# Kernel optimization log

Hardware: AMD Instinct MI355X
Metric: run time of the kernel (lower is better)

The kernel has to match this reference:

```python
import jax, jax.numpy as jnp
import numpy as np
from math import sqrt

EMA_W = 0.3  # ema_weight
LN_EPS = 1e-5


def setup_inputs() -> dict:
    key = jax.random.key(0)
    ks = jax.random.split(key, 16)
    B, L, H, E = 8, 1024, 8, 64
    d_ff, dp_rank = 2048, 8
    inp = {
        "queries": jax.random.normal(ks[0], (B, L, H, E), jnp.float32),
        "keys": jax.random.normal(ks[1], (B, L, H, E), jnp.float32),
        "values": jax.random.normal(ks[2], (B, L, H, E), jnp.float32),
        "attn_mask": jnp.zeros((B, 1, L, L), jnp.bool_),
        # dynamic-projection mlp: Linear(E, dp_rank)
        "mlp_w": jax.random.normal(ks[3], (E, dp_rank), jnp.float32) / sqrt(E),
        "mlp_b": jnp.zeros((dp_rank,), jnp.float32),
        # ff_1: Linear(E,d_ff) -> GELU -> Linear(d_ff,E)
        "ff1_w1": jax.random.normal(ks[4], (E, d_ff), jnp.float32) / sqrt(E),
        "ff1_b1": jnp.zeros((d_ff,), jnp.float32),
        "ff1_w2": jax.random.normal(ks[5], (d_ff, E), jnp.float32) / sqrt(d_ff),
        "ff1_b2": jnp.zeros((E,), jnp.float32),
        # ff_2
        "ff2_w1": jax.random.normal(ks[6], (E, d_ff), jnp.float32) / sqrt(E),
        "ff2_b1": jnp.zeros((d_ff,), jnp.float32),
        "ff2_w2": jax.random.normal(ks[7], (d_ff, E), jnp.float32) / sqrt(d_ff),
        "ff2_b2": jnp.zeros((E,), jnp.float32),
        # LayerNorm(E)
        "ln_w": jnp.ones((E,), jnp.float32),
        "ln_b": jnp.zeros((E,), jnp.float32),
    }
    return inp


def _dynamic_projection(src, mlp_w, mlp_b):
    # src: [B,L,H,E] -> softmax over dp_rank, then einsum 'blhe,blhr->blhe'
    sm = jax.nn.softmax(src @ mlp_w + mlp_b, axis=-1)  # [B,L,H,R]
    return jnp.einsum('blhe,blhr->blhe', src, sm)


def _ffn(x, w1, b1, w2, b2):
    return jax.nn.gelu(x @ w1 + b1, approximate=False) @ w2 + b2


def reference(queries, keys, values, attn_mask,
              mlp_w, mlp_b,
              ff1_w1, ff1_b1, ff1_w2, ff1_b2,
              ff2_w1, ff2_b1, ff2_w2, ff2_b2,
              ln_w, ln_b):
    E = queries.shape[-1]
    scale = 1.0 / sqrt(24.0)   # hardcoded in source
    scale1 = 1.0 / sqrt(E)

    dp_values = _dynamic_projection(values, mlp_w, mlp_b)
    dp_keys = _dynamic_projection(keys, mlp_w, mlp_b)

    # ema state starts at zeros every forward, so ema = (1-w) * x
    ema_queries = (1.0 - EMA_W) * queries
    ema_keys = (1.0 - EMA_W) * dp_keys

    # NOTE: source masks a scores tensor that is then overwritten; mask has
    # no effect on the output, so attn_mask is unused (kept for fidelity).
    scores = jnp.einsum('blhe,bshe->bhls', ema_queries, ema_keys)
    scores1 = jnp.einsum('blhe,bshe->bhls', queries, keys)

    A = jax.nn.softmax(scale * scores, axis=-1)    # dropout = identity (eval)
    A1 = jax.nn.softmax(scale1 * scores1, axis=-1)

    V = jnp.einsum('bhls,bshd->blhd', A, dp_values)
    V1 = jnp.einsum('bhls,bshd->blhd', A1, values)

    src = _ffn(V, ff1_w1, ff1_b1, ff1_w2, ff1_b2) + _ffn(V1, ff2_w1, ff2_b1, ff2_w2, ff2_b2)

    mu = jnp.mean(src, axis=-1, keepdims=True)
    var = jnp.mean(jnp.square(src - mu), axis=-1, keepdims=True)
    out = (src - mu) * jax.lax.rsqrt(var + LN_EPS) * ln_w + ln_b
    return out
```

## Files before the change

### kernel.cpp

```cpp
#include <hip/hip_runtime.h>

typedef _Float16 f16x8 __attribute__((ext_vector_type(8)));
typedef _Float16 f16x2 __attribute__((ext_vector_type(2)));
typedef float f32x4 __attribute__((ext_vector_type(4)));
typedef float f32x16 __attribute__((ext_vector_type(16)));
typedef unsigned short u16x8 __attribute__((ext_vector_type(8)));
typedef unsigned int u32x4 __attribute__((ext_vector_type(4)));

static __device__ __forceinline__ unsigned short f2h(float x) {
  return __builtin_bit_cast(unsigned short, (_Float16)x);
}
static __device__ __forceinline__ float h2f(unsigned short u) {
  return (float)__builtin_bit_cast(_Float16, u);
}

static __device__ __forceinline__ f16x2 gelu_pk(f16x2 x) {
  const f16x2 P4 = {(_Float16)4.0f, (_Float16)4.0f};
  const f16x2 N4 = {(_Float16)-4.0f, (_Float16)-4.0f};
  const f16x2 C1 = {(_Float16)0.392761f, (_Float16)0.392761f};
  const f16x2 C3 = {(_Float16)-0.0512736f, (_Float16)-0.0512736f};
  const f16x2 C5 = {(_Float16)0.00376322f, (_Float16)0.00376322f};
  const f16x2 C7 = {(_Float16)-0.000100287f, (_Float16)-0.000100287f};
  const f16x2 HF = {(_Float16)0.5f, (_Float16)0.5f};
  const f16x2 ONE = {(_Float16)1.0f, (_Float16)1.0f};
  const f16x2 ZRO = {(_Float16)0.0f, (_Float16)0.0f};
  f16x2 xc = __builtin_elementwise_max(__builtin_elementwise_min(x, P4), N4);
  f16x2 u = xc * xc;
  f16x2 p = __builtin_elementwise_fma(
      __builtin_elementwise_fma(__builtin_elementwise_fma(C7, u, C5), u, C3),
      u, C1);
  f16x2 q = __builtin_elementwise_fma(xc, p, HF);
  f16x2 qc = __builtin_elementwise_max(__builtin_elementwise_min(q, ONE), ZRO);
  return x * qc;
}

static __device__ __forceinline__ int sig16(int v) {
  return (v & ~12) | ((v & 4) << 1) | ((v & 8) >> 1);
}

__global__ __launch_bounds__(256) void k_prep(
    const float* __restrict__ vsrc, const float* __restrict__ ksrc,
    const float* __restrict__ w11, const float* __restrict__ w21,
    const float* __restrict__ w12, const float* __restrict__ w22,
    unsigned short* __restrict__ vtb, unsigned short* __restrict__ kf16,
    unsigned short* __restrict__ w1t1, unsigned short* __restrict__ w2t1,
    unsigned short* __restrict__ w1t2, unsigned short* __restrict__ w2t2) {
  int bid = blockIdx.x, tid = threadIdx.x;
  if (bid >= 1152) {
    int kb = bid - 1152, bh = kb >> 4, lt = kb & 15, b = bh >> 3, h = bh & 7;
    const float* src = ksrc + (((b * 1024 + lt * 64) * 8 + h) << 6);
    unsigned short* dst = kf16 + bh * 65536 + lt * 4096;
#pragma unroll
    for (int i = 0; i < 2; ++i) {
      int c = tid + i * 256, r = c >> 3, c8 = c & 7;
      const float* s = src + r * 512 + c8 * 8;
      f32x4 a = *(const f32x4*)s, b4 = *(const f32x4*)(s + 4);
      u16x8 vv;
#pragma unroll
      for (int j = 0; j < 4; ++j) { vv[j] = f2h(a[j]); vv[j + 4] = f2h(b4[j]); }
      int off = ((c8 >> 2) * 4 + (r >> 4)) * 512 + ((c8 & 3) * 16 + (r & 15)) * 8;
      *(u16x8*)(dst + off) = vv;
    }
    return;
  }
  __shared__ unsigned short t[64][72];
  const float* src; unsigned short* dst; int srs, drs = 0;
  bool isw2 = false, isv = false;
  if (bid < 1024) {
    int bh = bid >> 4, lt = bid & 15, b = bh >> 3, h = bh & 7;
    src = vsrc + (((b * 1024 + lt * 64) * 8 + h) << 6); srs = 512;
    dst = vtb + bh * 65536 + lt * 4096; isv = true;
  } else {
    int wb = bid - 1024, which = wb >> 5, ti = wb & 31;
    isw2 = (which & 1);
    if (which == 0)      { src = w11 + ti * 64;   srs = 2048; dst = w1t1 + ti * 4096; drs = 64; }
    else if (which == 1) { src = w21 + ti * 4096; srs = 64;   dst = w2t1 + ti * 64;   drs = 2048; }
    else if (which == 2) { src = w12 + ti * 64;   srs = 2048; dst = w1t2 + ti * 4096; drs = 64; }
    else                 { src = w22 + ti * 4096; srs = 64;   dst = w2t2 + ti * 64;   drs = 2048; }
  }
#pragma unroll
  for (int i = 0; i < 2; ++i) {
    int c = tid + i * 256, r = c >> 3, c0 = (c & 7) * 8;
    const float* s = src + r * srs + c0;
    int tr = isw2 ? sig16(r) : r;
#pragma unroll
    for (int j = 0; j < 8; ++j) t[c0 + j][tr] = f2h(s[j]);
  }
  __syncthreads();
#pragma unroll
  for (int i = 0; i < 2; ++i) {
    int c = tid + i * 256, r = c >> 3, c8 = c & 7;
    u16x8 vv;
#pragma unroll
    for (int j = 0; j < 8; ++j) vv[j] = t[r][c8 * 8 + j];
    int off = isv ? ((c8 >> 2) * 4 + (r >> 4)) * 512 + ((c8 & 3) * 16 + (r & 15)) * 8
                  : r * drs + c8 * 8;
    *(u16x8*)(dst + off) = vv;
  }
}

__global__ __launch_bounds__(64) __attribute__((amdgpu_waves_per_eu(1, 2)))
void k_attn(
    const float* __restrict__ q, const unsigned short* __restrict__ kf16,
    const unsigned short* __restrict__ vtb,
    unsigned short* __restrict__ Vo, unsigned short* __restrict__ V1o) {
  int bid = blockIdx.x;
  int swz = (bid & 7) * 256 + (bid >> 3);
  int bh = swz >> 5, rb = swz & 31;
  int b = bh >> 3, h = bh & 7;
  int lane = threadIdx.x & 63, t = lane & 15, g = lane >> 4;

  __shared__ unsigned short Pl[2][2048];

  f16x8 aq[2][2];
#pragma unroll
  for (int sub = 0; sub < 2; ++sub) {
    int row = rb * 32 + sub * 16 + t;
    const float* qp = q + ((b * 1024 + row) * 8 + h) * 64;
#pragma unroll
    for (int ks = 0; ks < 2; ++ks) {
      f32x4 q0 = *(const f32x4*)(qp + ks * 32 + g * 8);
      f32x4 q1 = *(const f32x4*)(qp + ks * 32 + g * 8 + 4);
      f16x8 a;
#pragma unroll
      for (int j = 0; j < 4; ++j) { a[j] = (_Float16)q0[j]; a[j + 4] = (_Float16)q1[j]; }
      aq[sub][ks] = a;
    }
  }

  const float scl[2] = {0.14429954f, 0.18033688f};
  float lsp[2][2][4];
  f32x4 o[2][2][4];
#pragma unroll
  for (int v = 0; v < 2; ++v)
#pragma unroll
    for (int sub = 0; sub < 2; ++sub)
#pragma unroll
      for (int i = 0; i < 4; ++i) {
        lsp[v][sub][i] = 0.f;
        o[v][sub][i] = (f32x4){0, 0, 0, 0};
      }

  const unsigned short* kfb = kf16 + bh * 65536;
  const unsigned short* vbase = vtb + bh * 65536;

  f16x8 bk[8];
#pragma unroll
  for (int fr = 0; fr < 8; ++fr)
    bk[fr] = *(const f16x8*)(kfb + fr * 512 + lane * 8);

#pragma unroll 1
  for (int kt = 0; kt < 16; ++kt) {
    f16x8 bv[8];
#pragma unroll
    for (int fr = 0; fr < 8; ++fr)
      bv[fr] = *(const f16x8*)(vbase + kt * 4096 + fr * 512 + lane * 8);

    f32x4 s[2][4];
#pragma unroll
    for (int sub = 0; sub < 2; ++sub)
#pragma unroll
      for (int nt = 0; nt < 4; ++nt) s[sub][nt] = (f32x4){0, 0, 0, 0};
#pragma unroll
    for (int ks = 0; ks < 2; ++ks)
#pragma unroll
      for (int sub = 0; sub < 2; ++sub)
#pragma unroll
        for (int nt = 0; nt < 4; ++nt)
          s[sub][nt] = __builtin_amdgcn_mfma_f32_16x16x32_f16(
              aq[sub][ks], bk[ks * 4 + nt], s[sub][nt], 0, 0, 0);

    if (kt < 15) {
#pragma unroll
      for (int fr = 0; fr < 8; ++fr)
        bk[fr] = *(const f16x8*)(kfb + (kt + 1) * 4096 + fr * 512 + lane * 8);
    }
    __builtin_amdgcn_sched_barrier(0);

#pragma unroll
    for (int v = 0; v < 2; ++v)
#pragma unroll
      for (int sub = 0; sub < 2; ++sub) {
        float pr[4][4];
#pragma unroll
        for (int nt = 0; nt < 4; ++nt)
#pragma unroll
          for (int reg = 0; reg < 4; ++reg)
            pr[nt][reg] = exp2f(s[sub][nt][reg] * scl[v]);
#pragma unroll
        for (int nt = 0; nt < 4; ++nt)
#pragma unroll
          for (int reg = 0; reg < 4; ++reg) {
            int r = g * 4 + reg, sc = nt * 16 + t;
            Pl[v][(sub * 16 + r) * 64 + ((((sc >> 3) ^ (r & 7)) << 3) | (sc & 7))] =
                f2h(pr[nt][reg]);
          }
#pragma unroll
        for (int reg = 0; reg < 4; ++reg)
          lsp[v][sub][reg] += (pr[0][reg] + pr[1][reg]) + (pr[2][reg] + pr[3][reg]);
      }
    asm volatile("s_waitcnt lgkmcnt(0)" ::: "memory");
#pragma unroll
    for (int v = 0; v < 2; ++v)
#pragma unroll
      for (int ks = 0; ks < 2; ++ks)
#pragma unroll
        for (int sub = 0; sub < 2; ++sub) {
          f16x8 ap = *(const f16x8*)&Pl[v][(sub * 16 + t) * 64 +
                                           (((ks * 4 + g) ^ (t & 7)) << 3)];
#pragma unroll
          for (int nt = 0; nt < 4; ++nt)
            o[v][sub][nt] = __builtin_amdgcn_mfma_f32_16x16x32_f16(
                ap, bv[ks * 4 + nt], o[v][sub][nt], 0, 0, 0);
        }
  }

#pragma unroll
  for (int v = 0; v < 2; ++v)
#pragma unroll
    for (int sub = 0; sub < 2; ++sub)
#pragma unroll
      for (int dd = 1; dd < 16; dd <<= 1)
#pragma unroll
        for (int reg = 0; reg < 4; ++reg)
          lsp[v][sub][reg] += __shfl_xor(lsp[v][sub][reg], dd);

#pragma unroll
  for (int sub = 0; sub < 2; ++sub)
#pragma unroll
    for (int nt = 0; nt < 4; ++nt)
#pragma unroll
      for (int reg = 0; reg < 4; ++reg) {
        int row = rb * 32 + sub * 16 + g * 4 + reg;
        int idx = ((b * 1024 + row) * 8 + h) * 64 + nt * 16 + t;
        float r0 = __builtin_amdgcn_rcpf(lsp[0][sub][reg]);
        float r1 = __builtin_amdgcn_rcpf(lsp[1][sub][reg]);
        Vo[idx]  = f2h(o[0][sub][nt][reg] * r0);
        V1o[idx] = f2h(o[1][sub][nt][reg] * r1);
      }
}

static __device__ __forceinline__ void compute_chunk(
    int j, const unsigned short* __restrict__ W1buf,
    const unsigned short* __restrict__ W2buf,
    const float* __restrict__ biasL, const f16x8 (&bx)[4],
    f32x16& acc0, f32x16& acc1, int t5, int hh) {
  f32x16 d0, d1;
#pragma unroll
  for (int rq = 0; rq < 4; ++rq) {
    f32x4 bb0 = *(const f32x4*)(biasL + j * 64 + rq * 8 + hh * 4);
    f32x4 bb1 = *(const f32x4*)(biasL + j * 64 + 32 + rq * 8 + hh * 4);
#pragma unroll
    for (int jj = 0; jj < 4; ++jj) { d0[rq * 4 + jj] = bb0[jj]; d1[rq * 4 + jj] = bb1[jj]; }
  }
#pragma unroll
  for (int ks = 0; ks < 4; ++ks) {
    int fr0 = t5;
    f16x8 aw0 = *(const f16x8*)&W1buf[fr0 * 64 + (((ks * 2 + hh) ^ (fr0 & 7)) << 3)];
    d0 = __builtin_amdgcn_mfma_f32_32x32x16_f16(aw0, bx[ks], d0, 0, 0, 0);
    int fr1 = 32 + t5;
    f16x8 aw1 = *(const f16x8*)&W1buf[fr1 * 64 + (((ks * 2 + hh) ^ (fr1 & 7)) << 3)];
    d1 = __builtin_amdgcn_mfma_f32_32x32x16_f16(aw1, bx[ks], d1, 0, 0, 0);
  }
#pragma unroll
  for (int g = 0; g < 4; ++g) {
    u32x4 av;
#pragma unroll
    for (int q = 0; q < 4; ++q) {
      int base = (g & 1) * 8 + 2 * q;
      float lo = (g < 2) ? d0[base] : d1[base];
      float hi = (g < 2) ? d0[base + 1] : d1[base + 1];
      f16x2 hx = __builtin_bit_cast(f16x2, __builtin_amdgcn_cvt_pkrtz(lo, hi));
      av[q] = __builtin_bit_cast(unsigned, gelu_pk(hx));
    }
    f16x8 hb = __builtin_bit_cast(f16x8, av);
    int er0 = t5;
    f16x8 wa0 = *(const f16x8*)&W2buf[er0 * 64 + (((g * 2 + hh) ^ (er0 & 7)) << 3)];
    acc0 = __builtin_amdgcn_mfma_f32_32x32x16_f16(wa0, hb, acc0, 0, 0, 0);
    int er1 = 32 + t5;
    f16x8 wa1 = *(const f16x8*)&W2buf[er1 * 64 + (((g * 2 + hh) ^ (er1 & 7)) << 3)];
    acc1 = __builtin_amdgcn_mfma_f32_32x32x16_f16(wa1, hb, acc1, 0, 0, 0);
  }
}

__global__ __launch_bounds__(256) void k_ffn(
    const unsigned short* __restrict__ Vo, const unsigned short* __restrict__ V1o,
    const unsigned short* __restrict__ w1ta, const unsigned short* __restrict__ w2ta,
    const unsigned short* __restrict__ w1tb, const unsigned short* __restrict__ w2tb,
    const float* __restrict__ b1a, const float* __restrict__ b1b,
    unsigned short* __restrict__ p0, unsigned short* __restrict__ p1,
    unsigned short* __restrict__ p2, unsigned short* __restrict__ p3) {
  int bid = blockIdx.x;
  int quar = bid >> 9, rb = bid & 511;
  int tid = threadIdx.x, w = tid >> 6, lane = tid & 63;
  int t5 = lane & 31, hh = lane >> 5;
  int rowbase = rb * 128 + w * 32;
  unsigned short* pout = (quar == 0) ? p0 : (quar == 1) ? p1 : (quar == 2) ? p2 : p3;

  __shared__ unsigned short W1c[4096];
  __shared__ unsigned short W2c[4096];
  __shared__ float biasL[2][512];

  if (tid < 128) {
    *(f32x4*)&biasL[0][tid * 4] = *(const f32x4*)(b1a + quar * 512 + tid * 4);
    *(f32x4*)&biasL[1][tid * 4] = *(const f32x4*)(b1b + quar * 512 + tid * 4);
  }

  f32x16 acc0, acc1;
#pragma unroll
  for (int i = 0; i < 16; ++i) { acc0[i] = 0.f; acc1[i] = 0.f; }

  int r0 = tid >> 3, c8 = tid & 7;
  int sw = (c8 ^ (r0 & 7)) << 3;

#pragma unroll 1
  for (int ffn = 0; ffn < 2; ++ffn) {
    const unsigned short* X = ffn ? V1o : Vo;
    const unsigned short* w1t = ffn ? w1tb : w1ta;
    const unsigned short* w2t = ffn ? w2tb : w2ta;
    f16x8 bx[4];
#pragma unroll
    for (int ks = 0; ks < 4; ++ks)
      bx[ks] = *(const f16x8*)(X + (rowbase + t5) * 64 + ks * 16 + hh * 8);

    int cbase = quar * 8;
    u16x8 ra0 = *(const u16x8*)(w1t + (cbase * 64 + r0) * 64 + c8 * 8);
    u16x8 ra1 = *(const u16x8*)(w1t + (cbase * 64 + r0 + 32) * 64 + c8 * 8);
    u16x8 rb0 = *(const u16x8*)(w2t + r0 * 2048 + cbase * 64 + c8 * 8);
    u16x8 rb1 = *(const u16x8*)(w2t + (r0 + 32) * 2048 + cbase * 64 + c8 * 8);

#pragma unroll 1
    for (int j = 0; j < 8; ++j) {
      __syncthreads();
      *(u16x8*)&W1c[r0 * 64 + sw] = ra0;
      *(u16x8*)&W2c[r0 * 64 + sw] = rb0;
      *(u16x8*)&W1c[(r0 + 32) * 64 + sw] = ra1;
      *(u16x8*)&W2c[(r0 + 32) * 64 + sw] = rb1;
      __syncthreads();
      if (j < 7) {
        int c1 = cbase + j + 1;
        ra0 = *(const u16x8*)(w1t + (c1 * 64 + r0) * 64 + c8 * 8);
        ra1 = *(const u16x8*)(w1t + (c1 * 64 + r0 + 32) * 64 + c8 * 8);
        rb0 = *(const u16x8*)(w2t + r0 * 2048 + c1 * 64 + c8 * 8);
        rb1 = *(const u16x8*)(w2t + (r0 + 32) * 2048 + c1 * 64 + c8 * 8);
      }
      compute_chunk(j, W1c, W2c, &biasL[ffn][0], bx, acc0, acc1, t5, hh);
    }
  }

  int orow = rowbase + t5;
#pragma unroll
  for (int q = 0; q < 8; ++q) {
    int e0 = (2 * q & 3) + 8 * (q >> 1) + 4 * hh;
    unsigned pa = __builtin_bit_cast(unsigned,
        __builtin_amdgcn_cvt_pkrtz(acc0[2 * q], acc0[2 * q + 1]));
    unsigned pb = __builtin_bit_cast(unsigned,
        __builtin_amdgcn_cvt_pkrtz(acc1[2 * q], acc1[2 * q + 1]));
    *(unsigned*)(pout + orow * 64 + e0) = pa;
    *(unsigned*)(pout + orow * 64 + 32 + e0) = pb;
  }
}

__global__ __launch_bounds__(256) void k_reduce(
    const unsigned short* __restrict__ p0, const unsigned short* __restrict__ p1,
    const unsigned short* __restrict__ p2, const unsigned short* __restrict__ p3,
    const float* __restrict__ b2a, const float* __restrict__ b2b,
    const float* __restrict__ lnw, const float* __restrict__ lnb,
    float* __restrict__ out) {
  int tid = threadIdx.x, w = tid >> 6, lane = tid & 63;
  float bias = b2a[lane] + b2b[lane];
  float lw = lnw[lane], lb = lnb[lane];
  int wid = blockIdx.x * 4 + w;
#pragma unroll 4
  for (int i = 0; i < 16; ++i) {
    int r = wid * 16 + i;
    int ix = r * 64 + lane;
    float v = (h2f(p0[ix]) + h2f(p1[ix])) + (h2f(p2[ix]) + h2f(p3[ix])) + bias;
    float s1 = v, s2 = v * v;
#pragma unroll
    for (int dd = 1; dd < 64; dd <<= 1) {
      s1 += __shfl_xor(s1, dd);
      s2 += __shfl_xor(s2, dd);
    }
    float mu = s1 * 0.015625f;
    float var = s2 * 0.015625f - mu * mu;
    out[ix] = (v - mu) * rsqrtf(var + 1e-5f) * lw + lb;
  }
}

extern "C" void kernel_launch(void* const* d_in, const int* in_sizes, int n_in,
                              void* d_out, int out_size, void* d_ws, size_t ws_size,
                              hipStream_t stream) {
  (void)in_sizes; (void)n_in; (void)out_size; (void)ws_size;
  const float* q   = (const float*)d_in[0];
  const float* k   = (const float*)d_in[1];
  const float* v   = (const float*)d_in[2];
  const float* w11 = (const float*)d_in[6];
  const float* b11 = (const float*)d_in[7];
  const float* w21 = (const float*)d_in[8];
  const float* b21 = (const float*)d_in[9];
  const float* w12 = (const float*)d_in[10];
  const float* b12 = (const float*)d_in[11];
  const float* w22 = (const float*)d_in[12];
  const float* b22 = (const float*)d_in[13];
  const float* lnw = (const float*)d_in[14];
  const float* lnb = (const float*)d_in[15];

  unsigned short* vtb  = (unsigned short*)d_ws;
  unsigned short* Vo   = vtb + 4194304;
  unsigned short* V1o  = Vo + 4194304;
  unsigned short* w1t1 = V1o + 4194304;
  unsigned short* w2t1 = w1t1 + 131072;
  unsigned short* w1t2 = w2t1 + 131072;
  unsigned short* w2t2 = w1t2 + 131072;
  unsigned short* part1 = w2t2 + 131072;
  unsigned short* kf16  = part1 + 4194304;
  unsigned short* part3 = kf16 + 4194304;
  unsigned short* part0 = vtb;
  unsigned short* part2 = kf16;

  k_prep<<<dim3(2176), dim3(256), 0, stream>>>(v, k, w11, w21, w12, w22,
                                               vtb, kf16, w1t1, w2t1, w1t2, w2t2);
  k_attn<<<dim3(2048), dim3(64), 0, stream>>>(q, kf16, vtb, Vo, V1o);
  k_ffn<<<dim3(2048), dim3(256), 0, stream>>>(Vo, V1o, w1t1, w2t1, w1t2, w2t2,
                                              b11, b12, part0, part1, part2, part3);
  k_reduce<<<dim3(1024), dim3(256), 0, stream>>>(part0, part1, part2, part3,
                                                 b21, b22, lnw, lnb, (float*)d_out);
}
```

Baseline: 216.4 us.

## Pre-swizzle FFN weights into MFMA fragment order and load directly from global

```diff
diff --git a/kernel.cpp b/kernel.cpp
--- a/kernel.cpp
+++ b/kernel.cpp
@@ -64,7 +64,7 @@
     return;
   }
   __shared__ unsigned short t[64][72];
-  const float* src; unsigned short* dst; int srs, drs = 0;
+  const float* src; unsigned short* dst; int srs;
   bool isw2 = false, isv = false;
   if (bid < 1024) {
     int bh = bid >> 4, lt = bid & 15, b = bh >> 3, h = bh & 7;
@@ -73,10 +73,10 @@
   } else {
     int wb = bid - 1024, which = wb >> 5, ti = wb & 31;
     isw2 = (which & 1);
-    if (which == 0)      { src = w11 + ti * 64;   srs = 2048; dst = w1t1 + ti * 4096; drs = 64; }
-    else if (which == 1) { src = w21 + ti * 4096; srs = 64;   dst = w2t1 + ti * 64;   drs = 2048; }
-    else if (which == 2) { src = w12 + ti * 64;   srs = 2048; dst = w1t2 + ti * 4096; drs = 64; }
-    else                 { src = w22 + ti * 4096; srs = 64;   dst = w2t2 + ti * 64;   drs = 2048; }
+    if (which == 0)      { src = w11 + ti * 64;   srs = 2048; dst = w1t1 + ti * 4096; }
+    else if (which == 1) { src = w21 + ti * 4096; srs = 64;   dst = w2t1 + ti * 4096; }
+    else if (which == 2) { src = w12 + ti * 64;   srs = 2048; dst = w1t2 + ti * 4096; }
+    else                 { src = w22 + ti * 4096; srs = 64;   dst = w2t2 + ti * 4096; }
   }
 #pragma unroll
   for (int i = 0; i < 2; ++i) {
@@ -94,7 +94,7 @@
 #pragma unroll
     for (int j = 0; j < 8; ++j) vv[j] = t[r][c8 * 8 + j];
     int off = isv ? ((c8 >> 2) * 4 + (r >> 4)) * 512 + ((c8 & 3) * 16 + (r & 15)) * 8
-                  : r * drs + c8 * 8;
+                  : ((c8 >> 1) * 2 + (r >> 5)) * 512 + ((c8 & 1) * 32 + (r & 31)) * 8;
     *(u16x8*)(dst + off) = vv;
   }
 }
@@ -238,49 +238,6 @@
         Vo[idx]  = f2h(o[0][sub][nt][reg] * r0);
         V1o[idx] = f2h(o[1][sub][nt][reg] * r1);
       }
-}
-
-static __device__ __forceinline__ void compute_chunk(
-    int j, const unsigned short* __restrict__ W1buf,
-    const unsigned short* __restrict__ W2buf,
-    const float* __restrict__ biasL, const f16x8 (&bx)[4],
-    f32x16& acc0, f32x16& acc1, int t5, int hh) {
-  f32x16 d0, d1;
-#pragma unroll
-  for (int rq = 0; rq < 4; ++rq) {
-    f32x4 bb0 = *(const f32x4*)(biasL + j * 64 + rq * 8 + hh * 4);
-    f32x4 bb1 = *(const f32x4*)(biasL + j * 64 + 32 + rq * 8 + hh * 4);
-#pragma unroll
-    for (int jj = 0; jj < 4; ++jj) { d0[rq * 4 + jj] = bb0[jj]; d1[rq * 4 + jj] = bb1[jj]; }
-  }
-#pragma unroll
-  for (int ks = 0; ks < 4; ++ks) {
-    int fr0 = t5;
-    f16x8 aw0 = *(const f16x8*)&W1buf[fr0 * 64 + (((ks * 2 + hh) ^ (fr0 & 7)) << 3)];
-    d0 = __builtin_amdgcn_mfma_f32_32x32x16_f16(aw0, bx[ks], d0, 0, 0, 0);
-    int fr1 = 32 + t5;
-    f16x8 aw1 = *(const f16x8*)&W1buf[fr1 * 64 + (((ks * 2 + hh) ^ (fr1 & 7)) << 3)];
-    d1 = __builtin_amdgcn_mfma_f32_32x32x16_f16(aw1, bx[ks], d1, 0, 0, 0);
-  }
-#pragma unroll
-  for (int g = 0; g < 4; ++g) {
-    u32x4 av;
-#pragma unroll
-    for (int q = 0; q < 4; ++q) {
-      int base = (g & 1) * 8 + 2 * q;
-      float lo = (g < 2) ? d0[base] : d1[base];
-      float hi = (g < 2) ? d0[base + 1] : d1[base + 1];
-      f16x2 hx = __builtin_bit_cast(f16x2, __builtin_amdgcn_cvt_pkrtz(lo, hi));
-      av[q] = __builtin_bit_cast(unsigned, gelu_pk(hx));
-    }
-    f16x8 hb = __builtin_bit_cast(f16x8, av);
-    int er0 = t5;
-    f16x8 wa0 = *(const f16x8*)&W2buf[er0 * 64 + (((g * 2 + hh) ^ (er0 & 7)) << 3)];
-    acc0 = __builtin_amdgcn_mfma_f32_32x32x16_f16(wa0, hb, acc0, 0, 0, 0);
-    int er1 = 32 + t5;
-    f16x8 wa1 = *(const f16x8*)&W2buf[er1 * 64 + (((g * 2 + hh) ^ (er1 & 7)) << 3)];
-    acc1 = __builtin_amdgcn_mfma_f32_32x32x16_f16(wa1, hb, acc1, 0, 0, 0);
-  }
 }
 
 __global__ __launch_bounds__(256) void k_ffn(
@@ -297,21 +254,16 @@
   int rowbase = rb * 128 + w * 32;
   unsigned short* pout = (quar == 0) ? p0 : (quar == 1) ? p1 : (quar == 2) ? p2 : p3;
 
-  __shared__ unsigned short W1c[4096];
-  __shared__ unsigned short W2c[4096];
   __shared__ float biasL[2][512];
-
   if (tid < 128) {
     *(f32x4*)&biasL[0][tid * 4] = *(const f32x4*)(b1a + quar * 512 + tid * 4);
     *(f32x4*)&biasL[1][tid * 4] = *(const f32x4*)(b1b + quar * 512 + tid * 4);
   }
+  __syncthreads();
 
   f32x16 acc0, acc1;
 #pragma unroll
   for (int i = 0; i < 16; ++i) { acc0[i] = 0.f; acc1[i] = 0.f; }
-
-  int r0 = tid >> 3, c8 = tid & 7;
-  int sw = (c8 ^ (r0 & 7)) << 3;
 
 #pragma unroll 1
   for (int ffn = 0; ffn < 2; ++ffn) {
@@ -323,28 +275,51 @@
     for (int ks = 0; ks < 4; ++ks)
       bx[ks] = *(const f16x8*)(X + (rowbase + t5) * 64 + ks * 16 + hh * 8);
 
-    int cbase = quar * 8;
-    u16x8 ra0 = *(const u16x8*)(w1t + (cbase * 64 + r0) * 64 + c8 * 8);
-    u16x8 ra1 = *(const u16x8*)(w1t + (cbase * 64 + r0 + 32) * 64 + c8 * 8);
-    u16x8 rb0 = *(const u16x8*)(w2t + r0 * 2048 + cbase * 64 + c8 * 8);
-    u16x8 rb1 = *(const u16x8*)(w2t + (r0 + 32) * 2048 + cbase * 64 + c8 * 8);
-
 #pragma unroll 1
     for (int j = 0; j < 8; ++j) {
-      __syncthreads();
-      *(u16x8*)&W1c[r0 * 64 + sw] = ra0;
-      *(u16x8*)&W2c[r0 * 64 + sw] = rb0;
-      *(u16x8*)&W1c[(r0 + 32) * 64 + sw] = ra1;
-      *(u16x8*)&W2c[(r0 + 32) * 64 + sw] = rb1;
-      __syncthreads();
-      if (j < 7) {
-        int c1 = cbase + j + 1;
-        ra0 = *(const u16x8*)(w1t + (c1 * 64 + r0) * 64 + c8 * 8);
-        ra1 = *(const u16x8*)(w1t + (c1 * 64 + r0 + 32) * 64 + c8 * 8);
-        rb0 = *(const u16x8*)(w2t + r0 * 2048 + c1 * 64 + c8 * 8);
-        rb1 = *(const u16x8*)(w2t + (r0 + 32) * 2048 + c1 * 64 + c8 * 8);
-      }
-      compute_chunk(j, W1c, W2c, &biasL[ffn][0], bx, acc0, acc1, t5, hh);
+      int c = quar * 8 + j;
+      const unsigned short* w1p = w1t + c * 4096;
+      const unsigned short* w2p = w2t + c * 4096;
+
+      f16x8 aw[8];
+#pragma unroll
+      for (int f = 0; f < 8; ++f)
+        aw[f] = *(const f16x8*)(w1p + f * 512 + lane * 8);
+
+      f32x16 d0, d1;
+#pragma unroll
+      for (int rq = 0; rq < 4; ++rq) {
+        f32x4 bb0 = *(const f32x4*)(&biasL[ffn][j * 64 + rq * 8 + hh * 4]);
+        f32x4 bb1 = *(const f32x4*)(&biasL[ffn][j * 64 + 32 + rq * 8 + hh * 4]);
+#pragma unroll
+        for (int jj = 0; jj < 4; ++jj) { d0[rq * 4 + jj] = bb0[jj]; d1[rq * 4 + jj] = bb1[jj]; }
+      }
+#pragma unroll
+      for (int ks = 0; ks < 4; ++ks) {
+        d0 = __builtin_amdgcn_mfma_f32_32x32x16_f16(aw[ks * 2 + 0], bx[ks], d0, 0, 0, 0);
+        d1 = __builtin_amdgcn_mfma_f32_32x32x16_f16(aw[ks * 2 + 1], bx[ks], d1, 0, 0, 0);
+      }
+
+      f16x8 wa[8];
+#pragma unroll
+      for (int f = 0; f < 8; ++f)
+        wa[f] = *(const f16x8*)(w2p + f * 512 + lane * 8);
+
+#pragma unroll
+      for (int g = 0; g < 4; ++g) {
+        u32x4 av;
+#pragma unroll
+        for (int q = 0; q < 4; ++q) {
+          int base = (g & 1) * 8 + 2 * q;
+          float lo = (g < 2) ? d0[base] : d1[base];
+          float hi = (g < 2) ? d0[base + 1] : d1[base + 1];
+          f16x2 hx = __builtin_bit_cast(f16x2, __builtin_amdgcn_cvt_pkrtz(lo, hi));
+          av[q] = __builtin_bit_cast(unsigned, gelu_pk(hx));
+        }
+        f16x8 hb = __builtin_bit_cast(f16x8, av);
+        acc0 = __builtin_amdgcn_mfma_f32_32x32x16_f16(wa[g * 2 + 0], hb, acc0, 0, 0, 0);
+        acc1 = __builtin_amdgcn_mfma_f32_32x32x16_f16(wa[g * 2 + 1], hb, acc1, 0, 0, 0);
+      }
     }
   }
 
```

New measurement: 218.8 us. No clear change (+1.1%).
